# Performance work log

Hardware: AMD Instinct MI355X
Metric: run time of the kernel (lower is better)

## Reference

```python
import jax, jax.numpy as jnp
import numpy as np

# Dims: S strings, B batch, D bond dim, N=784 input sites, P=2 phys dim, L=10 labels
S, B, D, N, P, L = 4, 64, 32, 784, 2, 10
HALF = N // 2  # 392 sites on each side of the label node


def setup_inputs() -> dict:
    key = jax.random.key(0)
    ks = jax.random.split(key, 6)
    # scale chosen so each transfer-matrix step keeps vector norm ~O(1)
    std = (3.0 / (2.0 * D)) ** 0.5
    inputs = jax.random.uniform(ks[0], (B, N, P), dtype=jnp.float32)
    A_first = jax.random.normal(ks[1], (S, D, P), dtype=jnp.float32) * std          # node 0
    A_left = jax.random.normal(ks[2], (S, HALF - 1, D, P, D), dtype=jnp.float32) * std   # nodes 1..391
    A_label = jax.random.normal(ks[3], (S, D, L, D), dtype=jnp.float32) * std       # node 392 (open label edge)
    A_right = jax.random.normal(ks[4], (S, HALF - 1, D, P, D), dtype=jnp.float32) * std  # nodes 393..783
    A_last = jax.random.normal(ks[5], (S, D, P), dtype=jnp.float32) * std           # node 784
    return {"inputs": inputs, "A_first": A_first, "A_left": A_left,
            "A_label": A_label, "A_right": A_right, "A_last": A_last}


def reference(inputs, A_first, A_left, A_label, A_right, A_last):
    x = inputs  # (B, N, P); original reshapes each sample to (784, 2)
    # Contract physical legs with inputs -> per-site transfer matrices, site-major for scan
    Ml = jnp.einsum('snipj,bnp->nsbij', A_left, x[:, 1:HALF])      # (391, S, B, D, D)
    v0 = jnp.einsum('sdp,bp->sbd', A_first, x[:, 0])               # (S, B, D)

    def step_left(v, M):
        return jnp.einsum('sbi,sbij->sbj', v, M), None
    v, _ = jax.lax.scan(step_left, v0, Ml)                          # (S, B, D)

    T = jnp.einsum('sbd,sdlj->sblj', v, A_label)                    # (S, B, L, D)

    Mr = jnp.einsum('snipj,bnp->nsbij', A_right, x[:, HALF:N - 1])  # (391, S, B, D, D)
    r0 = jnp.einsum('sdp,bp->sbd', A_last, x[:, N - 1])             # (S, B, D)

    def step_right(r, M):
        return jnp.einsum('sbij,sbj->sbi', M, r), None
    r, _ = jax.lax.scan(step_right, r0, Mr, reverse=True)           # (S, B, D)

    out_per_string = jnp.einsum('sblj,sbj->sbl', T, r)              # (S, B, L)
    # forward multiplies the per-string 10-vectors elementwise (init ones)
    return jnp.prod(out_per_string, axis=0)                         # (B, L)
```

## Files before the change

kernel.cpp:

```cpp
#include <hip/hip_runtime.h>
#include <stdint.h>

#define S 4
#define B 64
#define D 32
#define N 784
#define P 2
#define L 10
#define HALF 392
#define NSTEP 391
#define NPAIR 196
#define SLICE 4096

typedef float f4 __attribute__((ext_vector_type(4)));
typedef float f2 __attribute__((ext_vector_type(2)));

__device__ __forceinline__ float bcast(float v, int lane) {
    return __uint_as_float(__builtin_amdgcn_readlane(__float_as_uint(v), lane));
}

__global__ __launch_bounds__(256) void pair_kernel(
    const float* __restrict__ A_left, const float* __restrict__ A_right,
    const float* __restrict__ x,
    float* __restrict__ Wbuf, float* __restrict__ wtab)
{
    const int stream = blockIdx.x;
    const int t      = (NPAIR - 1) - blockIdx.y;
    const int side   = stream >> 2, s = stream & 3;
    __shared__ float sA[2048], sB[2048];
    const int tid = threadIdx.x;
    const bool leftover = (t == 195);

    const float* As = (side ? A_right : A_left) + (size_t)s * (NSTEP * 2048);
    int ia, ib;
    if (side == 0) { ia = 2 * t; ib = 2 * t + 1; }
    else           { ia = 389 - 2 * t; ib = 390 - 2 * t; }
    if (leftover)  { ia = side ? 0 : 390; ib = ia; }

    const float4* ga = (const float4*)(As + (size_t)ia * 2048);
    const float4* gb = (const float4*)(As + (size_t)ib * 2048);
    ((float4*)sA)[tid] = ga[tid]; ((float4*)sA)[tid + 256] = ga[tid + 256];
    ((float4*)sB)[tid] = gb[tid]; ((float4*)sB)[tid + 256] = gb[tid + 256];
    __syncthreads();

    const int c = tid >> 6, rest = tid & 63, ff = rest >> 1, eh = rest & 1;
    const int a = c & 1, bb = c >> 1;
    float out[16];

    if (!leftover) {
        if (side == 0) {
            float col[32];
            #pragma unroll
            for (int k = 0; k < 32; ++k) col[k] = sB[k * 64 + bb * 32 + ff];
            #pragma unroll
            for (int e0 = 0; e0 < 16; ++e0) {
                const int e = eh * 16 + e0; float acc = 0.f;
                #pragma unroll
                for (int k = 0; k < 32; ++k)
                    acc = fmaf(sA[e * 64 + a * 32 + k], col[k], acc);
                out[e0] = acc;
            }
        } else {
            float row[32];
            #pragma unroll
            for (int k = 0; k < 32; ++k) row[k] = sA[ff * 64 + a * 32 + k];
            #pragma unroll
            for (int e0 = 0; e0 < 16; ++e0) {
                const int e = eh * 16 + e0; float acc = 0.f;
                #pragma unroll
                for (int k = 0; k < 32; ++k)
                    acc = fmaf(row[k], sB[k * 64 + bb * 32 + e], acc);
                out[e0] = acc;
            }
        }
    } else {
        #pragma unroll
        for (int e0 = 0; e0 < 16; ++e0) {
            const int e = eh * 16 + e0;
            out[e0] = (side == 0) ? sA[e * 64 + a * 32 + ff]
                                  : sA[ff * 64 + a * 32 + e];
        }
    }

    float* Wt = Wbuf + ((size_t)stream * NPAIR + t) * SLICE;
    #pragma unroll
    for (int q0 = 0; q0 < 4; ++q0) {
        const int qq = eh * 4 + q0;
        float4 val = make_float4(out[q0 * 4 + 0], out[q0 * 4 + 1],
                                 out[q0 * 4 + 2], out[q0 * 4 + 3]);
        ((float4*)Wt)[(bb * 8 + qq) * 64 + a * 32 + ff] = val;
    }

    if (stream < 2 && tid < 64) {
        const int sd = stream;
        const float2* x2 = (const float2*)x;
        float2 xa, xb;
        if (!leftover) {
            int na, nb;
            if (sd == 0) { na = 2 * t + 1; nb = 2 * t + 2; }
            else         { int ma = 389 - 2 * t; na = HALF + ma; nb = na + 1; }
            xa = x2[(size_t)tid * N + na];
            xb = x2[(size_t)tid * N + nb];
        } else {
            xa = x2[(size_t)tid * N + (sd ? HALF : 391)];
            xb = make_float2(1.f, 0.f);
        }
        float4 w = make_float4(xa.x * xb.x, xa.y * xb.x, xa.x * xb.y, xa.y * xb.y);
        ((float4*)wtab)[((size_t)sd * 64 + tid) * NPAIR + t] = w;
    }
}

#define GLOADX4(dst, voff, base, off) \
    asm volatile("global_load_dwordx4 %0, %1, %2 offset:" #off \
                 : "=v"(dst) : "v"(voff), "s"(base))

#define ISSUE8(SL) do { \
    GLOADX4(SL##0, voff, base0, 0);    GLOADX4(SL##1, voff, base0, 1024); \
    GLOADX4(SL##2, voff, base0, 2048); GLOADX4(SL##3, voff, base0, 3072); \
    GLOADX4(SL##4, voff, base1, 0);    GLOADX4(SL##5, voff, base1, 1024); \
    GLOADX4(SL##6, voff, base1, 2048); GLOADX4(SL##7, voff, base1, 3072); \
    voff += 16384; \
} while (0)

#define WAITV(n) do { \
    asm volatile("s_waitcnt vmcnt(" #n ")" ::: "memory"); \
    __builtin_amdgcn_sched_barrier(0); \
} while (0)

#define WAITL(n) do { \
    asm volatile("s_waitcnt lgkmcnt(" #n ")" ::: "memory"); \
    __builtin_amdgcn_sched_barrier(0); \
} while (0)

#define CHUNK(Rq, EB) do { \
    const f2 l0 = __builtin_shufflevector(Rq, Rq, 0, 1); \
    const f2 l1 = __builtin_shufflevector(Rq, Rq, 2, 3); \
    f2 sa0, sa1, sb0, sb1; \
    sa0.x = bcast(v0, EB + 0); sa0.y = bcast(v0, EB + 1); \
    sa1.x = bcast(v0, EB + 2); sa1.y = bcast(v0, EB + 3); \
    sb0.x = bcast(v1, EB + 0); sb0.y = bcast(v1, EB + 1); \
    sb1.x = bcast(v1, EB + 2); sb1.y = bcast(v1, EB + 3); \
    QA0 = __builtin_elementwise_fma(l0, sa0, QA0); \
    QB0 = __builtin_elementwise_fma(l1, sa1, QB0); \
    QA1 = __builtin_elementwise_fma(l0, sb0, QA1); \
    QB1 = __builtin_elementwise_fma(l1, sb1, QB1); \
} while (0)

#define STEP(SL, WN, DO_ISSUE) do { \
    WAITV(WN); \
    f2 QA0 = {0.f,0.f}, QB0 = {0.f,0.f}, QA1 = {0.f,0.f}, QB1 = {0.f,0.f}; \
    CHUNK(SL##0, 0);  CHUNK(SL##1, 4);  CHUNK(SL##2, 8);  CHUNK(SL##3, 12); \
    CHUNK(SL##4, 16); CHUNK(SL##5, 20); CHUNK(SL##6, 24); CHUNK(SL##7, 28); \
    if (DO_ISSUE) { ISSUE8(SL); } \
    WAITL(0);   \
    const float sum0 = (QA0.x + QA0.y) + (QB0.x + QB0.y); \
    const float sum1 = (QA1.x + QA1.y) + (QB1.x + QB1.y); \
    float part0 = wreg.x * sum0; \
    float part1 = wreg.y * sum1; \
    part0 += __shfl_xor(part0, 32); \
    part1 += __shfl_xor(part1, 32); \
    f2 pp; pp.x = part0; pp.y = part1; \
    asm volatile("ds_write_b64 %0, %1" :: "v"(ewr), "v"(pp) : "memory"); \
    WAITL(0); \
    __builtin_amdgcn_s_barrier(); \
    f2 oth; \
    asm volatile("ds_read_b64 %0, %1" : "=v"(oth) : "v"(er)); \
    asm volatile("ds_read2_b32 %0, %1 offset0:0 offset1:4" : "=v"(wreg) : "v"(w_addr)); \
    w_addr += 32; ewr += ptog; er += ptog; ptog = -ptog; \
    WAITL(1);   \
    v0 = part0 + oth.x; \
    v1 = part1 + oth.y; \
} while (0)

__global__ __launch_bounds__(128, 1) void chain_kernel(
    const float* __restrict__ x,
    const float* __restrict__ A_first, const float* __restrict__ A_last,
    const float* __restrict__ Wbuf, const float* __restrict__ wtab,
    float* __restrict__ ws_v)
{
    __shared__ float4 lw[2 * (NPAIR + 2)];
    __shared__ f2 exch[2][2][32];

    const int tid  = threadIdx.x;
    const int w    = tid >> 6;
    const int lane = tid & 63;
    const int c2   = lane >> 5, f = lane & 31;
    const int blk  = blockIdx.x, stream = blk & 7;
    const int side = stream >> 2, s = stream & 3;
    const int bp   = blk >> 3;
    const int b0   = 2 * bp, b1 = 2 * bp + 1;

    const float4* wt4 = (const float4*)wtab;
    for (int i = tid; i < NPAIR; i += 128) {
        lw[2 * i]     = wt4[((size_t)side * 64 + b0) * NPAIR + i];
        lw[2 * i + 1] = wt4[((size_t)side * 64 + b1) * NPAIR + i];
    }
    __syncthreads();

    const float2* x2 = (const float2*)x;
    const int site0 = side ? (N - 1) : 0;
    const float2 af  = ((const float2*)(side ? A_last : A_first))[s * D + f];
    const float2 xx0 = x2[(size_t)b0 * N + site0];
    const float2 xx1 = x2[(size_t)b1 * N + site0];
    float v0 = fmaf(af.x, xx0.x, af.y * xx0.y);
    float v1 = fmaf(af.x, xx1.x, af.y * xx1.y);

    asm volatile("s_waitcnt vmcnt(0) lgkmcnt(0)" ::: "memory");
    __builtin_amdgcn_sched_barrier(0);

    const uint64_t wb = (uint64_t)((const char*)Wbuf
                      + (size_t)stream * (NPAIR * SLICE) * 4 + (size_t)w * 8192);
    const uint32_t wb_lo = __builtin_amdgcn_readfirstlane((uint32_t)wb);
    const uint32_t wb_hi = __builtin_amdgcn_readfirstlane((uint32_t)(wb >> 32));
    const uint64_t base0 = ((uint64_t)wb_hi << 32) | wb_lo;
    const uint64_t base1 = base0 + 4096;
    uint32_t voff = (uint32_t)lane * 16;

    uint32_t w_addr = (uint32_t)(uintptr_t)&lw[0] + (uint32_t)(c2 + 2 * w) * 4;
    uint32_t ewr = (uint32_t)(uintptr_t)&exch[0][w][f];
    uint32_t er  = (uint32_t)(uintptr_t)&exch[0][1 - w][f];
    int ptog = 512;

    f4 KA0,KA1,KA2,KA3,KA4,KA5,KA6,KA7;
    f4 KB0,KB1,KB2,KB3,KB4,KB5,KB6,KB7;
    f4 KC0,KC1,KC2,KC3,KC4,KC5,KC6,KC7;

    ISSUE8(KA); ISSUE8(KB); ISSUE8(KC);
    f2 wreg;
    asm volatile("ds_read2_b32 %0, %1 offset0:0 offset1:4" : "=v"(wreg) : "v"(w_addr));
    w_addr += 32;

    for (int k = 0; k < 64; ++k) {
        STEP(KA, 16, 1);
        STEP(KB, 16, 1);
        STEP(KC, 16, 1);
    }
    STEP(KA, 16, 1);
    STEP(KB, 16, 0);
    STEP(KC, 8,  0);
    STEP(KA, 0,  0);

    if (tid < 32) {
        ws_v[(side * S + s) * (B * D) + b0 * D + f] = v0;
        ws_v[(side * S + s) * (B * D) + b1 * D + f] = v1;
    }
}

__global__ __launch_bounds__(64) void chain_fb(
    const float* __restrict__ x, const float* __restrict__ A_first,
    const float* __restrict__ A_left, const float* __restrict__ A_right,
    const float* __restrict__ A_last, float* __restrict__ ws_v)
{
    const int blk = blockIdx.x, pair = blk & 7, b = blk >> 3;
    const int side = pair >> 2, s = pair & 3;
    const int lane = threadIdx.x, p = lane >> 5, j = lane & 31;
    const float* xb = x + b * (N * P);
    float v;
    if (side == 0) {
        v = fmaf(A_first[s*D*P + j*P + 0], xb[0], A_first[s*D*P + j*P + 1] * xb[1]);
        const float* Abase = A_left + (size_t)s * (NSTEP * D * P * D);
        for (int n = 1; n <= NSTEP; ++n) {
            const float* M = Abase + (n - 1) * (D * P * D) + p * D + j;
            const float x0 = xb[n*P], x1 = xb[n*P + 1];
            float t0 = 0.f, t1 = 0.f;
            #pragma unroll
            for (int i = 0; i < D; i += 2) {
                t0 = fmaf(bcast(v, i),     M[i * (P*D)],       t0);
                t1 = fmaf(bcast(v, i + 1), M[(i + 1) * (P*D)], t1);
            }
            const float t = t0 + t1, o = __shfl_xor(t, 32);
            v = (p == 0) ? fmaf(x0, t, x1 * o) : fmaf(x1, t, x0 * o);
        }
    } else {
        v = fmaf(A_last[s*D*P + j*P + 0], xb[(N-1)*P], A_last[s*D*P + j*P + 1] * xb[(N-1)*P + 1]);
        const float* Abase = A_right + (size_t)s * (NSTEP * D * P * D);
        for (int m = NSTEP - 1; m >= 0; --m) {
            const float4* R4 = (const float4*)(Abase + m * (D*P*D) + j * (P*D) + p * D);
            const float x0 = xb[(HALF+m)*P], x1 = xb[(HALF+m)*P + 1];
            float t0 = 0.f, t1 = 0.f;
            #pragma unroll
            for (int q = 0; q < 8; ++q) {
                const float4 rv = R4[q];
                t0 = fmaf(rv.x, bcast(v, 4*q+0), t0);
                t1 = fmaf(rv.y, bcast(v, 4*q+1), t1);
                t0 = fmaf(rv.z, bcast(v, 4*q+2), t0);
                t1 = fmaf(rv.w, bcast(v, 4*q+3), t1);
            }
            const float t = t0 + t1, o = __shfl_xor(t, 32);
            v = (p == 0) ? fmaf(x0, t, x1 * o) : fmaf(x1, t, x0 * o);
        }
    }
    if (p == 0) ws_v[(side*S + s)*(B*D) + b*D + j] = v;
}

__global__ __launch_bounds__(64) void label_prod_kernel(
    const float* __restrict__ ws_v, const float* __restrict__ A_label,
    float* __restrict__ out)
{
    const int b = blockIdx.x;
    const int lane = threadIdx.x, h = lane >> 5, j = lane & 31;
    float pr0 = 1.f, pr1 = 1.f, pr2 = 1.f, pr3 = 1.f, pr4 = 1.f;

    #pragma unroll
    for (int s = 0; s < S; ++s) {
        const float vj = ws_v[(0 * S + s) * (B * D) + b * D + j];
        const float rj = ws_v[(1 * S + s) * (B * D) + b * D + j];
        #pragma unroll
        for (int q = 0; q < 5; ++q) {
            const int l = h * 5 + q;
            float w = 0.f;
            #pragma unroll
            for (int d = 0; d < D; ++d)
                w = fmaf(bcast(vj, d), A_label[((s * D + d) * L + l) * D + j], w);
            float c = w * rj;
            c += __shfl_xor(c, 1); c += __shfl_xor(c, 2); c += __shfl_xor(c, 4);
            c += __shfl_xor(c, 8); c += __shfl_xor(c, 16);
            if (q == 0) pr0 *= c; else if (q == 1) pr1 *= c;
            else if (q == 2) pr2 *= c; else if (q == 3) pr3 *= c; else pr4 *= c;
        }
    }
    if (j == 0) {
        out[b * L + h * 5 + 0] = pr0;
        out[b * L + h * 5 + 1] = pr1;
        out[b * L + h * 5 + 2] = pr2;
        out[b * L + h * 5 + 3] = pr3;
        out[b * L + h * 5 + 4] = pr4;
    }
}

extern "C" void kernel_launch(void* const* d_in, const int* in_sizes, int n_in,
                              void* d_out, int out_size, void* d_ws, size_t ws_size,
                              hipStream_t stream) {
    const float* x       = (const float*)d_in[0];
    const float* A_first = (const float*)d_in[1];
    const float* A_left  = (const float*)d_in[2];
    const float* A_label = (const float*)d_in[3];
    const float* A_right = (const float*)d_in[4];
    const float* A_last  = (const float*)d_in[5];
    float* out = (float*)d_out;

    float* ws_v = (float*)d_ws;
    float* wtab = ws_v + 2 * S * B * D;
    float* Wbuf = wtab + 2 * 64 * NPAIR * 4;
    const size_t need = (size_t)(16384 + 100352 + 8 * NPAIR * SLICE) * 4;

    if (ws_size >= need) {
        pair_kernel<<<dim3(8, NPAIR), dim3(256), 0, stream>>>(A_left, A_right, x, Wbuf, wtab);
        chain_kernel<<<dim3(256), dim3(128), 0, stream>>>(x, A_first, A_last, Wbuf, wtab, ws_v);
    } else {
        chain_fb<<<dim3(2 * S * B), dim3(64), 0, stream>>>(x, A_first, A_left, A_right, A_last, ws_v);
    }
    label_prod_kernel<<<dim3(B), dim3(64), 0, stream>>>(ws_v, A_label, out);
}
```

Measured before the change: 121.5 us.

## Process one batch sample per chain block and double the grid

The chain kernel now handles a single batch element per block instead of two, launching 512 blocks instead of 256. The per-step math, the LDS exchange and the weight table are halved, and register prefetch drops from triple to double buffering. The pair kernel's block ordering is also reversed. The aim is a shorter serial critical path per step and more CUs working in parallel. The cost is that each pair-matrix slice is streamed from memory twice as often, and each step has less prefetch depth to hide load latency.

```diff
diff --git a/kernel.cpp b/kernel.cpp
--- a/kernel.cpp
+++ b/kernel.cpp
@@ -25,7 +25,7 @@
     float* __restrict__ Wbuf, float* __restrict__ wtab)
 {
     const int stream = blockIdx.x;
-    const int t      = (NPAIR - 1) - blockIdx.y;
+    const int t      = blockIdx.y;
     const int side   = stream >> 2, s = stream & 3;
     __shared__ float sA[2048], sB[2048];
     const int tid = threadIdx.x;
@@ -132,54 +132,48 @@
     __builtin_amdgcn_sched_barrier(0); \
 } while (0)
 
-#define CHUNK(Rq, EB) do { \
+#define FQ(Rq, QA, QB, EB) do { \
     const f2 l0 = __builtin_shufflevector(Rq, Rq, 0, 1); \
     const f2 l1 = __builtin_shufflevector(Rq, Rq, 2, 3); \
-    f2 sa0, sa1, sb0, sb1; \
+    f2 sa0, sa1; \
     sa0.x = bcast(v0, EB + 0); sa0.y = bcast(v0, EB + 1); \
+    QA = __builtin_elementwise_fma(l0, sa0, QA); \
     sa1.x = bcast(v0, EB + 2); sa1.y = bcast(v0, EB + 3); \
-    sb0.x = bcast(v1, EB + 0); sb0.y = bcast(v1, EB + 1); \
-    sb1.x = bcast(v1, EB + 2); sb1.y = bcast(v1, EB + 3); \
-    QA0 = __builtin_elementwise_fma(l0, sa0, QA0); \
-    QB0 = __builtin_elementwise_fma(l1, sa1, QB0); \
-    QA1 = __builtin_elementwise_fma(l0, sb0, QA1); \
-    QB1 = __builtin_elementwise_fma(l1, sb1, QB1); \
+    QB = __builtin_elementwise_fma(l1, sa1, QB); \
 } while (0)
 
 #define STEP(SL, WN, DO_ISSUE) do { \
     WAITV(WN); \
-    f2 QA0 = {0.f,0.f}, QB0 = {0.f,0.f}, QA1 = {0.f,0.f}, QB1 = {0.f,0.f}; \
-    CHUNK(SL##0, 0);  CHUNK(SL##1, 4);  CHUNK(SL##2, 8);  CHUNK(SL##3, 12); \
-    CHUNK(SL##4, 16); CHUNK(SL##5, 20); CHUNK(SL##6, 24); CHUNK(SL##7, 28); \
+    f2 QA = {0.f, 0.f}, QB = {0.f, 0.f}; \
+    FQ(SL##0, QA, QB, 0);  FQ(SL##1, QA, QB, 4); \
+    FQ(SL##2, QA, QB, 8);  FQ(SL##3, QA, QB, 12); \
+    FQ(SL##4, QA, QB, 16); FQ(SL##5, QA, QB, 20); \
+    FQ(SL##6, QA, QB, 24); FQ(SL##7, QA, QB, 28); \
     if (DO_ISSUE) { ISSUE8(SL); } \
     WAITL(0);   \
-    const float sum0 = (QA0.x + QA0.y) + (QB0.x + QB0.y); \
-    const float sum1 = (QA1.x + QA1.y) + (QB1.x + QB1.y); \
-    float part0 = wreg.x * sum0; \
-    float part1 = wreg.y * sum1; \
-    part0 += __shfl_xor(part0, 32); \
-    part1 += __shfl_xor(part1, 32); \
-    f2 pp; pp.x = part0; pp.y = part1; \
-    asm volatile("ds_write_b64 %0, %1" :: "v"(ewr), "v"(pp) : "memory"); \
+    const float part = wreg * ((QA.x + QA.y) + (QB.x + QB.y)); \
+    const float pw   = part + __shfl_xor(part, 32); \
+    asm volatile("ds_write_b32 %0, %1" :: "v"(ewr), "v"(pw) : "memory"); \
     WAITL(0); \
     __builtin_amdgcn_s_barrier(); \
-    f2 oth; \
-    asm volatile("ds_read_b64 %0, %1" : "=v"(oth) : "v"(er)); \
-    asm volatile("ds_read2_b32 %0, %1 offset0:0 offset1:4" : "=v"(wreg) : "v"(w_addr)); \
-    w_addr += 32; ewr += ptog; er += ptog; ptog = -ptog; \
+    float oth; \
+    asm volatile("ds_read_b32 %0, %1" : "=v"(oth) : "v"(er)); \
+    asm volatile("ds_read_b32 %0, %1" : "=v"(wreg) : "v"(w_addr)); \
+    w_addr += 16; \
     WAITL(1);   \
-    v0 = part0 + oth.x; \
-    v1 = part1 + oth.y; \
-} while (0)
-
-__global__ __launch_bounds__(128, 1) void chain_kernel(
+    v0 = pw + oth; \
+    ewr += ptog; er += ptog; ptog = -ptog; \
+} while (0)
+
+__global__ __attribute__((amdgpu_waves_per_eu(1, 1))) __launch_bounds__(128, 1)
+void chain_kernel(
     const float* __restrict__ x,
     const float* __restrict__ A_first, const float* __restrict__ A_last,
     const float* __restrict__ Wbuf, const float* __restrict__ wtab,
     float* __restrict__ ws_v)
 {
-    __shared__ float4 lw[2 * (NPAIR + 2)];
-    __shared__ f2 exch[2][2][32];
+    __shared__ float4 lw[NPAIR + 2];
+    __shared__ float  exch[2][2][32];
 
     const int tid  = threadIdx.x;
     const int w    = tid >> 6;
@@ -187,23 +181,18 @@
     const int c2   = lane >> 5, f = lane & 31;
     const int blk  = blockIdx.x, stream = blk & 7;
     const int side = stream >> 2, s = stream & 3;
-    const int bp   = blk >> 3;
-    const int b0   = 2 * bp, b1 = 2 * bp + 1;
+    const int b    = blk >> 3;
 
     const float4* wt4 = (const float4*)wtab;
-    for (int i = tid; i < NPAIR; i += 128) {
-        lw[2 * i]     = wt4[((size_t)side * 64 + b0) * NPAIR + i];
-        lw[2 * i + 1] = wt4[((size_t)side * 64 + b1) * NPAIR + i];
-    }
+    for (int i = tid; i < NPAIR; i += 128)
+        lw[i] = wt4[((size_t)side * 64 + b) * NPAIR + i];
     __syncthreads();
 
     const float2* x2 = (const float2*)x;
     const int site0 = side ? (N - 1) : 0;
     const float2 af  = ((const float2*)(side ? A_last : A_first))[s * D + f];
-    const float2 xx0 = x2[(size_t)b0 * N + site0];
-    const float2 xx1 = x2[(size_t)b1 * N + site0];
+    const float2 xx0 = x2[(size_t)b * N + site0];
     float v0 = fmaf(af.x, xx0.x, af.y * xx0.y);
-    float v1 = fmaf(af.x, xx1.x, af.y * xx1.y);
 
     asm volatile("s_waitcnt vmcnt(0) lgkmcnt(0)" ::: "memory");
     __builtin_amdgcn_sched_barrier(0);
@@ -219,31 +208,26 @@
     uint32_t w_addr = (uint32_t)(uintptr_t)&lw[0] + (uint32_t)(c2 + 2 * w) * 4;
     uint32_t ewr = (uint32_t)(uintptr_t)&exch[0][w][f];
     uint32_t er  = (uint32_t)(uintptr_t)&exch[0][1 - w][f];
-    int ptog = 512;
+    int ptog = 256;
 
     f4 KA0,KA1,KA2,KA3,KA4,KA5,KA6,KA7;
     f4 KB0,KB1,KB2,KB3,KB4,KB5,KB6,KB7;
-    f4 KC0,KC1,KC2,KC3,KC4,KC5,KC6,KC7;
-
-    ISSUE8(KA); ISSUE8(KB); ISSUE8(KC);
-    f2 wreg;
-    asm volatile("ds_read2_b32 %0, %1 offset0:0 offset1:4" : "=v"(wreg) : "v"(w_addr));
-    w_addr += 32;
-
-    for (int k = 0; k < 64; ++k) {
-        STEP(KA, 16, 1);
-        STEP(KB, 16, 1);
-        STEP(KC, 16, 1);
-    }
-    STEP(KA, 16, 1);
-    STEP(KB, 16, 0);
-    STEP(KC, 8,  0);
-    STEP(KA, 0,  0);
-
-    if (tid < 32) {
-        ws_v[(side * S + s) * (B * D) + b0 * D + f] = v0;
-        ws_v[(side * S + s) * (B * D) + b1 * D + f] = v1;
-    }
+
+    ISSUE8(KA);
+    ISSUE8(KB);
+    float wreg;
+    asm volatile("ds_read_b32 %0, %1" : "=v"(wreg) : "v"(w_addr));
+    w_addr += 16;
+
+    for (int k = 0; k < 97; ++k) {
+        STEP(KA, 8, 1);
+        STEP(KB, 8, 1);
+    }
+    STEP(KA, 8, 0);
+    STEP(KB, 0, 0);
+
+    if (tid < 32)
+        ws_v[(side * S + s) * (B * D) + b * D + f] = v0;
 }
 
 __global__ __launch_bounds__(64) void chain_fb(
@@ -346,7 +330,7 @@
 
     if (ws_size >= need) {
         pair_kernel<<<dim3(8, NPAIR), dim3(256), 0, stream>>>(A_left, A_right, x, Wbuf, wtab);
-        chain_kernel<<<dim3(256), dim3(128), 0, stream>>>(x, A_first, A_last, Wbuf, wtab, ws_v);
+        chain_kernel<<<dim3(512), dim3(128), 0, stream>>>(x, A_first, A_last, Wbuf, wtab, ws_v);
     } else {
         chain_fb<<<dim3(2 * S * B), dim3(64), 0, stream>>>(x, A_first, A_left, A_right, A_last, ws_v);
     }
```

New measurement: 120.8 us. Within noise of the previous version (-0.5%).
